# Optimization experiments

Measured on AMD Instinct MI355X. Metric: run time of the kernel, lower is better.

The kernel has to match this reference:

```python
import jax, jax.numpy as jnp
import numpy as np

N_NODES = 100000
N_EDGES = 1600000
IN_DIM = 512
HID = 64
OUT_DIM = 5


def _gcn_conv(x, row, col, w, W, b, n_nodes):
    """PyG GCNConv: h = x @ W; out[col] += norm * h[row]; out += b.
    norm = deg^-1/2[row] * w * deg^-1/2[col], deg from edge weights scattered on col,
    with self-loops (weight 1) already appended by caller."""
    h = x @ W  # [N, F_out]
    deg = jax.ops.segment_sum(w, col, num_segments=n_nodes)  # [N]
    dinv = jnp.where(deg > 0, jax.lax.rsqrt(deg), 0.0)
    norm = dinv[row] * w * dinv[col]  # [E']
    msg = h[row] * norm[:, None]  # [E', F_out] edge-wise gather + scale
    out = jax.ops.segment_sum(msg, col, num_segments=n_nodes)  # scatter-add
    return out + b


def setup_inputs() -> dict:
    key = jax.random.key(0)
    ks = jax.random.split(key, 10)
    x = jax.random.normal(ks[0], (N_NODES, IN_DIM), dtype=jnp.float32)
    edge_index = jax.random.randint(ks[1], (2, N_EDGES), 0, N_NODES, dtype=jnp.int32)
    edge_attr = jax.random.uniform(ks[2], (N_EDGES,), dtype=jnp.float32)
    # Glorot-ish init for params
    W1 = jax.random.normal(ks[3], (IN_DIM, HID), dtype=jnp.float32) * (1.0 / np.sqrt(IN_DIM))
    b1 = jnp.zeros((HID,), dtype=jnp.float32)
    W2 = jax.random.normal(ks[4], (HID, HID), dtype=jnp.float32) * (1.0 / np.sqrt(HID))
    b2 = jnp.zeros((HID,), dtype=jnp.float32)
    Wfc = jax.random.normal(ks[5], (HID, OUT_DIM), dtype=jnp.float32) * (1.0 / np.sqrt(HID))
    bfc = jnp.zeros((OUT_DIM,), dtype=jnp.float32)
    return {"x": x, "edge_index": edge_index, "edge_attr": edge_attr,
            "W1": W1, "b1": b1, "W2": W2, "b2": b2, "Wfc": Wfc, "bfc": bfc}


def reference(x, edge_index, edge_attr, W1, b1, W2, b2, Wfc, bfc):
    n = x.shape[0]
    loop = jnp.arange(n, dtype=edge_index.dtype)
    row = jnp.concatenate([edge_index[0], loop])  # source nodes + self-loops
    col = jnp.concatenate([edge_index[1], loop])  # target nodes + self-loops
    w = jnp.concatenate([edge_attr, jnp.ones((n,), dtype=edge_attr.dtype)])
    h = jax.nn.relu(_gcn_conv(x, row, col, w, W1, b1, n))
    # dropout(p=0.5) is identity in eval/reference mode
    h = jax.nn.relu(_gcn_conv(h, row, col, w, W2, b2, n))
    return h @ Wfc + bfc
```

## Files before the change

### kernel.cpp

```cpp
#include <hip/hip_runtime.h>

#define HID 64
#define OUTD 5
#define BCAP 16384
#define PART_CHUNK 4096
#define CSTRIDE 16

typedef __attribute__((ext_vector_type(8))) short bf16x8;
typedef __attribute__((ext_vector_type(4))) float f32x4;

__device__ inline void split_bf16(float x, short& hi, short& lo) {
    unsigned u = __float_as_uint(x);
    unsigned h = u >> 16;
    float hf = __uint_as_float(h << 16);
    float lof = x - hf;
    unsigned l = __float_as_uint(lof) >> 16;
    hi = (short)h; lo = (short)l;
}

__device__ inline ushort f2bf(float x) {
    unsigned u = __float_as_uint(x);
    u += 0x7fffu + ((u >> 16) & 1u);
    return (ushort)(u >> 16);
}

__global__ void k_prep(const float* __restrict__ W1, const float* __restrict__ W2,
                       short* __restrict__ w1hi, short* __restrict__ w1lo,
                       short* __restrict__ w2hi, short* __restrict__ w2lo,
                       int* __restrict__ gcursor, int nbuck,
                       int* __restrict__ binCnt, int* __restrict__ binCur) {
    int gid = blockIdx.x * blockDim.x + threadIdx.x;
    if (gid < nbuck) gcursor[gid * CSTRIDE] = 0;
    if (gid < 64) { binCnt[gid * CSTRIDE] = 0; binCur[gid * CSTRIDE] = 0; }
    if (gid >= 32768 + 4096) return;
    int which = (gid >= 32768);
    int g = which ? gid - 32768 : gid;
    const float* W = which ? W2 : W1;
    short* ph = which ? w2hi : w1hi;
    short* pl = which ? w2lo : w1lo;
    int b = g & 7, lane = (g >> 3) & 63, c = (g >> 9) & 3, s = g >> 11;
    int k = s * 32 + 8 * (lane >> 4) + b;
    int j = c * 16 + (lane & 15);
    float x = W[k * 64 + j];
    short hi, lo; split_bf16(x, hi, lo);
    ph[g] = hi; pl[g] = lo;
}

__device__ inline void gemm1_body(const float* __restrict__ A,
                                  const short* __restrict__ whi,
                                  const short* __restrict__ wlo,
                                  ushort* __restrict__ C, int M, int bid, int tid,
                                  float* __restrict__ As) {
    const int K = 512;
    int lane = tid & 63;
    int wave = tid >> 6;
    int r0 = bid * 128;

    const bf16x8* bh = (const bf16x8*)whi + lane;
    const bf16x8* bl = (const bf16x8*)wlo + lane;

    f32x4 acc[2][4];
    #pragma unroll
    for (int r = 0; r < 2; r++)
        #pragma unroll
        for (int c = 0; c < 4; c++) acc[r][c] = (f32x4){0.f, 0.f, 0.f, 0.f};

    int lr0 = wave * 32 + (lane & 15);
    int lr1 = lr0 + 16;
    int cb = 2 * (lane >> 4);

    for (int s = 0; s < 16; s++) {
        int k0 = s * 32;
        __syncthreads();
        #pragma unroll
        for (int i = 0; i < 4; i++) {
            int sl = i * 256 + tid;
            int row = sl >> 3, c4 = sl & 7;
            int gr = r0 + row; if (gr >= M) gr = M - 1;
            float4 v = *(const float4*)(A + (size_t)gr * K + k0 + c4 * 4);
            *(float4*)&As[(size_t)(row * 8 + (c4 ^ (row & 7))) * 4] = v;
        }
        __syncthreads();

        float4 x0 = *(const float4*)&As[(size_t)(lr0 * 8 + ((cb)     ^ (lr0 & 7))) * 4];
        float4 x1 = *(const float4*)&As[(size_t)(lr0 * 8 + ((cb + 1) ^ (lr0 & 7))) * 4];
        float4 y0 = *(const float4*)&As[(size_t)(lr1 * 8 + ((cb)     ^ (lr1 & 7))) * 4];
        float4 y1 = *(const float4*)&As[(size_t)(lr1 * 8 + ((cb + 1) ^ (lr1 & 7))) * 4];
        float xs[8] = {x0.x, x0.y, x0.z, x0.w, x1.x, x1.y, x1.z, x1.w};
        float ys[8] = {y0.x, y0.y, y0.z, y0.w, y1.x, y1.y, y1.z, y1.w};
        bf16x8 ah0, al0, ah1, al1;
        #pragma unroll
        for (int e = 0; e < 8; e++) {
            short h, l;
            split_bf16(xs[e], h, l); ah0[e] = h; al0[e] = l;
            split_bf16(ys[e], h, l); ah1[e] = h; al1[e] = l;
        }
        #pragma unroll
        for (int c = 0; c < 4; c++) {
            bf16x8 wh = bh[(s * 4 + c) * 64];
            bf16x8 wl = bl[(s * 4 + c) * 64];
            acc[0][c] = __builtin_amdgcn_mfma_f32_16x16x32_bf16(ah0, wh, acc[0][c], 0, 0, 0);
            acc[0][c] = __builtin_amdgcn_mfma_f32_16x16x32_bf16(ah0, wl, acc[0][c], 0, 0, 0);
            acc[0][c] = __builtin_amdgcn_mfma_f32_16x16x32_bf16(al0, wh, acc[0][c], 0, 0, 0);
            acc[1][c] = __builtin_amdgcn_mfma_f32_16x16x32_bf16(ah1, wh, acc[1][c], 0, 0, 0);
            acc[1][c] = __builtin_amdgcn_mfma_f32_16x16x32_bf16(ah1, wl, acc[1][c], 0, 0, 0);
            acc[1][c] = __builtin_amdgcn_mfma_f32_16x16x32_bf16(al1, wh, acc[1][c], 0, 0, 0);
        }
    }

    int wr0 = r0 + wave * 32;
    #pragma unroll
    for (int r = 0; r < 2; r++) {
        #pragma unroll
        for (int reg = 0; reg < 4; reg++) {
            int grow = wr0 + r * 16 + 4 * (lane >> 4) + reg;
            if (grow < M) {
                #pragma unroll
                for (int c = 0; c < 4; c++)
                    C[(size_t)grow * 64 + c * 16 + (lane & 15)] = f2bf(acc[r][c][reg]);
            }
        }
    }
}

__global__ __launch_bounds__(256) void k_fused1(const float* __restrict__ x,
                                                const short* __restrict__ w1hi,
                                                const short* __restrict__ w1lo,
                                                ushort* __restrict__ h1, int M, int gGemm,
                                                const int* __restrict__ row,
                                                const int* __restrict__ col,
                                                const float* __restrict__ ea,
                                                int* __restrict__ gcursor,
                                                int2* __restrict__ bucket_mem,
                                                int nbuck, int E) {
    __shared__ __align__(16) char ldsbuf[128 * 32 * 4];
    int bid = blockIdx.x;
    int t = threadIdx.x;
    if (bid < gGemm) {
        gemm1_body(x, w1hi, w1lo, h1, M, bid, t, (float*)ldsbuf);
        return;
    }
    int* hist = (int*)ldsbuf;
    int* basearr = (int*)ldsbuf + 256;
    int e0 = (bid - gGemm) * PART_CHUNK;
    if (t < nbuck) hist[t] = 0;
    __syncthreads();
    int cols[PART_CHUNK / 256];
    #pragma unroll
    for (int i = 0; i < PART_CHUNK / 256; i++) {
        int e = e0 + t + i * 256;
        cols[i] = (e < E) ? col[e] : -1;
        if (cols[i] >= 0) atomicAdd(&hist[cols[i] >> 9], 1);
    }
    __syncthreads();
    if (t < nbuck) {
        basearr[t] = atomicAdd(&gcursor[t * CSTRIDE], hist[t]);
        hist[t] = 0;
    }
    __syncthreads();
    #pragma unroll
    for (int i = 0; i < PART_CHUNK / 256; i++) {
        int e = e0 + t + i * 256;
        if (e < E) {
            int c = cols[i];
            int b = c >> 9;
            int pos = basearr[b] + atomicAdd(&hist[b], 1);
            if (pos < BCAP) {
                int pack = ((c & 511) << 17) | row[e];
                bucket_mem[(size_t)b * BCAP + pos] = make_int2(pack, __float_as_int(ea[e]));
            }
        }
    }
}

__global__ __launch_bounds__(256) void k_build(const int* __restrict__ gcursor,
                                               const int2* __restrict__ bucket_mem,
                                               int2* __restrict__ edges,
                                               int2* __restrict__ nodemeta,
                                               float* __restrict__ dinv,
                                               int* __restrict__ used,
                                               int* __restrict__ binCnt, int n) {
    __shared__ int hcnt[512];
    __shared__ int hoff[512];
    __shared__ float hdeg[512];
    __shared__ int ps[256];
    __shared__ int hbin[64];
    int b = blockIdx.x;
    int t = threadIdx.x;
    int cntb = gcursor[b * CSTRIDE]; if (cntb > BCAP) cntb = BCAP;
    const int2* bm = bucket_mem + (size_t)b * BCAP;

    #pragma unroll
    for (int l = t; l < 512; l += 256) { hcnt[l] = 0; hdeg[l] = 0.f; }
    if (t < 64) hbin[t] = 0;
    __syncthreads();
    for (int i = t; i < cntb; i += 256) atomicAdd(&hcnt[bm[i].x >> 17], 1);
    __syncthreads();
    int c0 = hcnt[2 * t], c1 = hcnt[2 * t + 1];
    int q0 = (c0 + 15) & ~15; if (q0 < 16) q0 = 16;
    int q1 = (c1 + 15) & ~15; if (q1 < 16) q1 = 16;
    ps[t] = q0 + q1;
    __syncthreads();
    for (int o = 1; o < 256; o <<= 1) {
        int v = (t >= o) ? ps[t - o] : 0;
        __syncthreads();
        ps[t] += v;
        __syncthreads();
    }
    int excl = ps[t] - (q0 + q1);
    hoff[2 * t] = excl;
    hoff[2 * t + 1] = excl + q0;
    if (t == 255) used[b] = ps[255];
    __syncthreads();
    #pragma unroll
    for (int l = t; l < 512; l += 256) hcnt[l] = 0;
    __syncthreads();
    for (int i = t; i < cntb; i += 256) {
        int2 eM = bm[i];
        int local = eM.x >> 17;
        int src = eM.x & 0x1FFFF;
        int p = hoff[local] + atomicAdd(&hcnt[local], 1);
        edges[(size_t)b * BCAP + p] = make_int2(src, eM.y);
        atomicAdd(&hdeg[local], __int_as_float(eM.y));
    }
    __syncthreads();
    #pragma unroll
    for (int l = t; l < 512; l += 256) {
        int node = b * 512 + l;
        if (node < n) {
            int cnt = hcnt[l];
            int pc = (cnt + 15) & ~15; if (pc < 16) pc = 16;
            for (int p2 = cnt; p2 < pc; p2++)
                edges[(size_t)b * BCAP + hoff[l] + p2] = make_int2(node, 0);
            nodemeta[node] = make_int2(b * BCAP + hoff[l], pc);
            dinv[node] = rsqrtf(hdeg[l] + 1.0f);
            int bin = pc >> 4; if (bin > 63) bin = 63;
            atomicAdd(&hbin[bin], 1);
        }
    }
    __syncthreads();
    if (t < 64 && hbin[t] > 0) atomicAdd(&binCnt[t * CSTRIDE], hbin[t]);
}

__global__ void k_norm2(int2* __restrict__ edges, const float* __restrict__ dinv,
                        const int* __restrict__ used, int n, int nbuck, int gNorm,
                        const int* __restrict__ binCnt, int* __restrict__ binBase) {
    if (blockIdx.x == (unsigned)gNorm) {
        if (threadIdx.x == 0) {
            int acc = 0;
            for (int i = 0; i < 64; i++) { binBase[i] = acc; acc += binCnt[i * CSTRIDE]; }
        }
        return;
    }
    int gid = blockIdx.x * blockDim.x + threadIdx.x;
    int b = gid >> 14;
    if (b >= nbuck) return;
    int slot = gid & (BCAP - 1);
    if (slot >= used[b]) return;
    size_t idx = (size_t)b * BCAP + slot;
    int2 c = edges[idx];
    if ((unsigned)c.x < (unsigned)n) {
        c.y = __float_as_int(dinv[c.x] * __int_as_float(c.y));
        edges[idx] = c;
    }
}

__global__ void k_scatter(const int2* __restrict__ nodemeta, const int* __restrict__ binBase,
                          int* __restrict__ binCur, int* __restrict__ perm, int n) {
    __shared__ int lh[64];
    __shared__ int gb[64];
    int t = threadIdx.x;
    if (t < 64) lh[t] = 0;
    __syncthreads();
    int i = blockIdx.x * 256 + t;
    int bin = 0, r = 0;
    bool v = (i < n);
    if (v) {
        int pc = nodemeta[i].y;
        bin = pc >> 4; if (bin > 63) bin = 63;
        r = atomicAdd(&lh[bin], 1);
    }
    __syncthreads();
    if (t < 64) gb[t] = (lh[t] > 0) ? atomicAdd(&binCur[t * CSTRIDE], lh[t]) : 0;
    __syncthreads();
    if (v) perm[binBase[bin] + gb[bin] + r] = i;
}

template<int FC>
__global__ void k_gather4(const ushort* __restrict__ h, const int2* __restrict__ nodemeta,
                          const int2* __restrict__ edges, const float* __restrict__ dinv,
                          const int* __restrict__ perm,
                          const float* __restrict__ bias, const float* __restrict__ Wfc,
                          const float* __restrict__ bfc, ushort* __restrict__ outb,
                          float* __restrict__ outf, int n) {
    int gw = (blockIdx.x * blockDim.x + threadIdx.x) >> 6;
    int lane = threadIdx.x & 63;
    int s = lane & 15;
    int idx = gw * 4 + (lane >> 4);
    bool valid = (idx < n);
    if (!valid) idx = n - 1;
    int node = perm[idx];

    int2 meta = nodemeta[node];
    int cnt = meta.y;
    const int2* seg = edges + meta.x;
    uint2 self_u = *(const uint2*)&h[(size_t)node * 64 + 4 * s];
    float dvc = dinv[node];
    int mc = max(cnt, __shfl_xor(cnt, 16));
    mc = max(mc, __shfl_xor(mc, 32));

    float a0 = 0.f, a1 = 0.f, a2 = 0.f, a3 = 0.f;
    for (int i = 0; i < mc; i += 16) {
        int base = (i < cnt) ? i : (cnt - 16);
        float live = (i < cnt) ? 1.f : 0.f;
        int4 m[8];
        #pragma unroll
        for (int q = 0; q < 8; q++) m[q] = *(const int4*)(seg + base + 2 * q);
        uint2 v[16];
        #pragma unroll
        for (int q = 0; q < 8; q++) {
            v[2 * q]     = *(const uint2*)&h[(size_t)m[q].x * 64 + 4 * s];
            v[2 * q + 1] = *(const uint2*)&h[(size_t)m[q].z * 64 + 4 * s];
        }
        #pragma unroll
        for (int q = 0; q < 8; q++) {
            float w0 = __int_as_float(m[q].y) * live;
            float w1 = __int_as_float(m[q].w) * live;
            uint2 va = v[2 * q], vb = v[2 * q + 1];
            a0 += w0 * __uint_as_float(va.x << 16);
            a1 += w0 * __uint_as_float(va.x & 0xffff0000u);
            a2 += w0 * __uint_as_float(va.y << 16);
            a3 += w0 * __uint_as_float(va.y & 0xffff0000u);
            a0 += w1 * __uint_as_float(vb.x << 16);
            a1 += w1 * __uint_as_float(vb.x & 0xffff0000u);
            a2 += w1 * __uint_as_float(vb.y << 16);
            a3 += w1 * __uint_as_float(vb.y & 0xffff0000u);
        }
    }

    float4 bv = *(const float4*)&bias[4 * s];
    float dd = dvc * dvc;
    float r0 = fmaxf(dvc * a0 + dd * __uint_as_float(self_u.x << 16) + bv.x, 0.f);
    float r1 = fmaxf(dvc * a1 + dd * __uint_as_float(self_u.x & 0xffff0000u) + bv.y, 0.f);
    float r2 = fmaxf(dvc * a2 + dd * __uint_as_float(self_u.y << 16) + bv.z, 0.f);
    float r3 = fmaxf(dvc * a3 + dd * __uint_as_float(self_u.y & 0xffff0000u) + bv.w, 0.f);

    if (FC == 0) {
        if (valid) {
            uint lo = ((uint)f2bf(r1) << 16) | (uint)f2bf(r0);
            uint hi = ((uint)f2bf(r3) << 16) | (uint)f2bf(r2);
            *(uint2*)&outb[(size_t)node * 64 + 4 * s] = make_uint2(lo, hi);
        }
    } else {
        #pragma unroll
        for (int j = 0; j < OUTD; j++) {
            float p = r0 * Wfc[(4 * s) * OUTD + j] + r1 * Wfc[(4 * s + 1) * OUTD + j]
                    + r2 * Wfc[(4 * s + 2) * OUTD + j] + r3 * Wfc[(4 * s + 3) * OUTD + j];
            #pragma unroll
            for (int o = 1; o <= 8; o <<= 1) p += __shfl_xor(p, o);
            if (s == j && valid) outf[(size_t)node * OUTD + j] = p + bfc[j];
        }
    }
}

__global__ __launch_bounds__(256) void k_gemm2(const ushort* __restrict__ A,
                                               const short* __restrict__ whi,
                                               const short* __restrict__ wlo,
                                               ushort* __restrict__ C, int M) {
    int tid = threadIdx.x;
    int lane = tid & 63;
    int wave = tid >> 6;
    int r0 = blockIdx.x * 128 + wave * 32;

    int ar0 = r0 + (lane & 15);      if (ar0 >= M) ar0 = M - 1;
    int ar1 = r0 + 16 + (lane & 15); if (ar1 >= M) ar1 = M - 1;
    const ushort* pa0 = A + (size_t)ar0 * 64 + 8 * (lane >> 4);
    const ushort* pa1 = A + (size_t)ar1 * 64 + 8 * (lane >> 4);
    const bf16x8* bh = (const bf16x8*)whi + lane;
    const bf16x8* bl = (const bf16x8*)wlo + lane;

    f32x4 acc[2][4];
    #pragma unroll
    for (int r = 0; r < 2; r++)
        #pragma unroll
        for (int c = 0; c < 4; c++) acc[r][c] = (f32x4){0.f, 0.f, 0.f, 0.f};

    #pragma unroll
    for (int s = 0; s < 2; s++) {
        bf16x8 a0 = *(const bf16x8*)(pa0 + s * 32);
        bf16x8 a1 = *(const bf16x8*)(pa1 + s * 32);
        #pragma unroll
        for (int c = 0; c < 4; c++) {
            bf16x8 wh = bh[(s * 4 + c) * 64];
            bf16x8 wl = bl[(s * 4 + c) * 64];
            acc[0][c] = __builtin_amdgcn_mfma_f32_16x16x32_bf16(a0, wh, acc[0][c], 0, 0, 0);
            acc[0][c] = __builtin_amdgcn_mfma_f32_16x16x32_bf16(a0, wl, acc[0][c], 0, 0, 0);
            acc[1][c] = __builtin_amdgcn_mfma_f32_16x16x32_bf16(a1, wh, acc[1][c], 0, 0, 0);
            acc[1][c] = __builtin_amdgcn_mfma_f32_16x16x32_bf16(a1, wl, acc[1][c], 0, 0, 0);
        }
    }

    #pragma unroll
    for (int r = 0; r < 2; r++) {
        #pragma unroll
        for (int reg = 0; reg < 4; reg++) {
            int grow = r0 + r * 16 + 4 * (lane >> 4) + reg;
            if (grow < M) {
                #pragma unroll
                for (int c = 0; c < 4; c++)
                    C[(size_t)grow * 64 + c * 16 + (lane & 15)] = f2bf(acc[r][c][reg]);
            }
        }
    }
}

extern "C" void kernel_launch(void* const* d_in, const int* in_sizes, int n_in,
                              void* d_out, int out_size, void* d_ws, size_t ws_size,
                              hipStream_t stream) {
    const float* x   = (const float*)d_in[0];
    const int*   ei  = (const int*)d_in[1];
    const float* ea  = (const float*)d_in[2];
    const float* W1  = (const float*)d_in[3];
    const float* b1  = (const float*)d_in[4];
    const float* W2  = (const float*)d_in[5];
    const float* b2  = (const float*)d_in[6];
    const float* Wfc = (const float*)d_in[7];
    const float* bfc = (const float*)d_in[8];

    const int N = in_sizes[0] / 512;
    const int E = in_sizes[1] / 2;
    const int nbuck = (N + 511) >> 9;

    const int* row = ei;
    const int* col = ei + E;

    uintptr_t p = (uintptr_t)d_ws;
    auto carve = [&](size_t bytes) -> void* {
        void* r = (void*)p;
        p += (bytes + 255) & ~(size_t)255;
        return r;
    };
    int*    gcursor    = (int*)carve((size_t)nbuck * CSTRIDE * 4);
    int*    used       = (int*)carve((size_t)nbuck * 4);
    int*    binCnt     = (int*)carve(64 * CSTRIDE * 4);
    int*    binCur     = (int*)carve(64 * CSTRIDE * 4);
    int*    binBase    = (int*)carve(64 * 4);
    int*    perm       = (int*)carve((size_t)N * 4);
    float*  dinv       = (float*)carve((size_t)N * 4);
    int2*   nodemeta   = (int2*)carve((size_t)N * 8);
    int2*   bucket_mem = (int2*)carve((size_t)nbuck * BCAP * 8);
    int2*   edges      = (int2*)carve((size_t)nbuck * BCAP * 8);
    short*  w1hi       = (short*)carve(32768 * 2);
    short*  w1lo       = (short*)carve(32768 * 2);
    short*  w2hi       = (short*)carve(4096 * 2);
    short*  w2lo       = (short*)carve(4096 * 2);
    ushort* hbuf       = (ushort*)carve((size_t)N * 64 * 2);
    ushort* abuf       = (ushort*)carve((size_t)N * 64 * 2);
    (void)ws_size;

    const int B = 256;
    int gGemm = (N + 127) / 128;
    int gPart = (E + PART_CHUNK - 1) / PART_CHUNK;
    int gNorm = nbuck * (BCAP / B);
    int gGath = (((N + 3) / 4) * 64 + B - 1) / B;
    int gScat = (N + B - 1) / B;
    int gPrep = (32768 + 4096 + B - 1) / B;

    k_prep<<<gPrep, B, 0, stream>>>(W1, W2, w1hi, w1lo, w2hi, w2lo,
                                    gcursor, nbuck, binCnt, binCur);
    k_fused1<<<gGemm + gPart, B, 0, stream>>>(x, w1hi, w1lo, hbuf, N, gGemm,
                                              row, col, ea, gcursor, bucket_mem, nbuck, E);
    k_build<<<nbuck, B, 0, stream>>>(gcursor, bucket_mem, edges, nodemeta,
                                     dinv, used, binCnt, N);
    k_norm2<<<gNorm + 1, B, 0, stream>>>(edges, dinv, used, N, nbuck, gNorm,
                                         binCnt, binBase);
    k_scatter<<<gScat, B, 0, stream>>>(nodemeta, binBase, binCur, perm, N);
    k_gather4<0><<<gGath, B, 0, stream>>>(hbuf, nodemeta, edges, dinv, perm, b1,
                                          nullptr, nullptr, abuf, nullptr, N);
    k_gemm2<<<gGemm, B, 0, stream>>>(abuf, w2hi, w2lo, hbuf, N);
    k_gather4<1><<<gGath, B, 0, stream>>>(hbuf, nodemeta, edges, dinv, perm, b2,
                                          Wfc, bfc, nullptr, (float*)d_out, N);
}
```

Measured before the change: 230.8 us.

## Double-buffer LDS tiles and prefetch next A slice into registers in gemm1

The GEMM1 main loop now loads the next 32-column slice of x into registers while MFMAs run on the current LDS tile, then writes it into a second LDS buffer. This replaces two barriers per step with one and overlaps global loads with compute. In exchange, LDS use per block doubles to 32 KB, which may reduce occupancy, and register pressure rises.

```diff
diff --git a/kernel.cpp b/kernel.cpp
--- a/kernel.cpp
+++ b/kernel.cpp
@@ -52,6 +52,7 @@
                                   ushort* __restrict__ C, int M, int bid, int tid,
                                   float* __restrict__ As) {
     const int K = 512;
+    const int TILE = 128 * 32;
     int lane = tid & 63;
     int wave = tid >> 6;
     int r0 = bid * 128;
@@ -69,23 +70,36 @@
     int lr1 = lr0 + 16;
     int cb = 2 * (lane >> 4);
 
+    int srow[4], sc4[4], sofs[4];
+    const float* gbase[4];
+    #pragma unroll
+    for (int i = 0; i < 4; i++) {
+        int sl = i * 256 + tid;
+        srow[i] = sl >> 3; sc4[i] = sl & 7;
+        sofs[i] = (srow[i] * 8 + (sc4[i] ^ (srow[i] & 7))) * 4;
+        int gr = r0 + srow[i]; if (gr >= M) gr = M - 1;
+        gbase[i] = A + (size_t)gr * K + sc4[i] * 4;
+    }
+
+    float4 rg[4];
+    #pragma unroll
+    for (int i = 0; i < 4; i++) rg[i] = *(const float4*)(gbase[i]);
+    #pragma unroll
+    for (int i = 0; i < 4; i++) *(float4*)&As[sofs[i]] = rg[i];
+    __syncthreads();
+
     for (int s = 0; s < 16; s++) {
-        int k0 = s * 32;
-        __syncthreads();
-        #pragma unroll
-        for (int i = 0; i < 4; i++) {
-            int sl = i * 256 + tid;
-            int row = sl >> 3, c4 = sl & 7;
-            int gr = r0 + row; if (gr >= M) gr = M - 1;
-            float4 v = *(const float4*)(A + (size_t)gr * K + k0 + c4 * 4);
-            *(float4*)&As[(size_t)(row * 8 + (c4 ^ (row & 7))) * 4] = v;
-        }
-        __syncthreads();
-
-        float4 x0 = *(const float4*)&As[(size_t)(lr0 * 8 + ((cb)     ^ (lr0 & 7))) * 4];
-        float4 x1 = *(const float4*)&As[(size_t)(lr0 * 8 + ((cb + 1) ^ (lr0 & 7))) * 4];
-        float4 y0 = *(const float4*)&As[(size_t)(lr1 * 8 + ((cb)     ^ (lr1 & 7))) * 4];
-        float4 y1 = *(const float4*)&As[(size_t)(lr1 * 8 + ((cb + 1) ^ (lr1 & 7))) * 4];
+        float* cur = As + (s & 1) * TILE;
+        if (s < 15) {
+            int k0 = (s + 1) * 32;
+            #pragma unroll
+            for (int i = 0; i < 4; i++) rg[i] = *(const float4*)(gbase[i] + k0);
+        }
+
+        float4 x0 = *(const float4*)&cur[(lr0 * 8 + ((cb)     ^ (lr0 & 7))) * 4];
+        float4 x1 = *(const float4*)&cur[(lr0 * 8 + ((cb + 1) ^ (lr0 & 7))) * 4];
+        float4 y0 = *(const float4*)&cur[(lr1 * 8 + ((cb)     ^ (lr1 & 7))) * 4];
+        float4 y1 = *(const float4*)&cur[(lr1 * 8 + ((cb + 1) ^ (lr1 & 7))) * 4];
         float xs[8] = {x0.x, x0.y, x0.z, x0.w, x1.x, x1.y, x1.z, x1.w};
         float ys[8] = {y0.x, y0.y, y0.z, y0.w, y1.x, y1.y, y1.z, y1.w};
         bf16x8 ah0, al0, ah1, al1;
@@ -106,6 +120,13 @@
             acc[1][c] = __builtin_amdgcn_mfma_f32_16x16x32_bf16(ah1, wl, acc[1][c], 0, 0, 0);
             acc[1][c] = __builtin_amdgcn_mfma_f32_16x16x32_bf16(al1, wh, acc[1][c], 0, 0, 0);
         }
+
+        if (s < 15) {
+            float* nxt = As + ((s + 1) & 1) * TILE;
+            #pragma unroll
+            for (int i = 0; i < 4; i++) *(float4*)&nxt[sofs[i]] = rg[i];
+        }
+        __syncthreads();
     }
 
     int wr0 = r0 + wave * 32;
@@ -133,7 +154,7 @@
                                                 int* __restrict__ gcursor,
                                                 int2* __restrict__ bucket_mem,
                                                 int nbuck, int E) {
-    __shared__ __align__(16) char ldsbuf[128 * 32 * 4];
+    __shared__ __align__(16) char ldsbuf[2 * 128 * 32 * 4];
     int bid = blockIdx.x;
     int t = threadIdx.x;
     if (bid < gGemm) {
```

After: 249.8 us. 1.08x slower.
